# Kernel tuning notes

Hardware: AMD Instinct MI355X
Metric: run time of the kernel (lower is better)

Reference implementation:

```python
import jax, jax.numpy as jnp
import numpy as np

N_NODES = 50000
N_EDGES = 800000
D = 128


def gin_layer(x, edge_index, edge_attr, ee1, ee2, W1, b1, W2, b2):
    # PyG default flow source_to_target: x_j = x[edge_index[0]], aggregate at edge_index[1]
    src, dst = edge_index[0], edge_index[1]
    edge_emb = ee1[edge_attr[:, 0]] + ee2[edge_attr[:, 1]]           # [E, D]
    msg = x[src] + edge_emb                                          # [E, D]
    aggr = jax.ops.segment_sum(msg, dst, num_segments=x.shape[0])    # [N, D]
    h = jax.nn.relu(aggr @ W1 + b1)                                  # [N, 2D]
    return h @ W2 + b2                                               # [N, out]


def setup_inputs() -> dict:
    key = jax.random.key(0)
    ks = jax.random.split(key, 16)
    s = 1.0 / np.sqrt(D)
    inp = {
        "x": jax.random.normal(ks[0], (N_NODES, D), jnp.float32),
        "edge_index": jax.random.randint(ks[1], (2, N_EDGES), 0, N_NODES, dtype=jnp.int32),
        "edge_attr": jax.random.randint(ks[2], (N_EDGES, 2), 0, 3, dtype=jnp.int32),
        "ee1_0": jax.random.normal(ks[3], (6, D), jnp.float32) * s,
        "ee2_0": jax.random.normal(ks[4], (3, D), jnp.float32) * s,
        "W1_0": jax.random.normal(ks[5], (D, 2 * D), jnp.float32) * s,
        "b1_0": jnp.zeros((2 * D,), jnp.float32),
        "W2_0": jax.random.normal(ks[6], (2 * D, D), jnp.float32) * s,
        "b2_0": jnp.zeros((D,), jnp.float32),
        "ee1_1": jax.random.normal(ks[7], (6, D), jnp.float32) * s,
        "ee2_1": jax.random.normal(ks[8], (3, D), jnp.float32) * s,
        "W1_1": jax.random.normal(ks[9], (D, 2 * D), jnp.float32) * s,
        "b1_1": jnp.zeros((2 * D,), jnp.float32),
        "W2_1": jax.random.normal(ks[10], (2 * D, D), jnp.float32) * s,
        "b2_1": jnp.zeros((D,), jnp.float32),
    }
    return inp


def reference(x, edge_index, edge_attr, ee1_0, ee2_0, W1_0, b1_0, W2_0, b2_0,
              ee1_1, ee2_1, W1_1, b1_1, W2_1, b2_1):
    h = gin_layer(x, edge_index, edge_attr, ee1_0, ee2_0, W1_0, b1_0, W2_0, b2_0)
    h = jax.nn.relu(h)  # activation between GNN layers
    out = gin_layer(h, edge_index, edge_attr, ee1_1, ee2_1, W1_1, b1_1, W2_1, b2_1)
    return out  # jk='last'
```

## Files before the change

### kernel.cpp

```cpp
#include <hip/hip_runtime.h>

typedef __attribute__((ext_vector_type(8))) short s16x8;
typedef __attribute__((ext_vector_type(4))) float f32x4;
typedef unsigned short u16;
typedef unsigned char u8;
typedef unsigned long long u64;

#define D_FEAT 128
#define TILE1 4096

__device__ __forceinline__ u16 f2bf(float f) {
    unsigned u = __builtin_bit_cast(unsigned, f);
    u = u + 0x7fffu + ((u >> 16) & 1u);
    return (u16)(u >> 16);
}

__global__ __launch_bounds__(256) void prep_kernel(
        const float4* __restrict__ X4, u16* __restrict__ xb, int n4, int nbA,
        const int* __restrict__ dst, int* __restrict__ ghist, int E, int nb1, int bins,
        const float* __restrict__ ee1_0, const float* __restrict__ ee2_0,
        const float* __restrict__ ee1_1, const float* __restrict__ ee2_1,
        float* __restrict__ emb,
        const float* __restrict__ W1_0, const float* __restrict__ W2_0,
        const float* __restrict__ W1_1, const float* __restrict__ W2_1,
        u16* __restrict__ wout) {
    __shared__ int h[256];
    const int t = threadIdx.x;
    int b = blockIdx.x;

    if (b < nbA) {
        for (int i = b * 256 + t; i < n4; i += nbA * 256) {
            float4 v = X4[i];
            uint2 p;
            p.x = (unsigned)f2bf(v.x) | ((unsigned)f2bf(v.y) << 16);
            p.y = (unsigned)f2bf(v.z) | ((unsigned)f2bf(v.w) << 16);
            *(uint2*)(xb + (size_t)i * 4) = p;
        }
        return;
    }
    b -= nbA;
    if (b < nb1) {
        h[t] = 0;
        __syncthreads();
        const int base = b * TILE1;
        #pragma unroll
        for (int j = 0; j < TILE1 / 256; ++j) {
            int e = base + j * 256 + t;
            if (e < E) atomicAdd(&h[dst[e] >> 8], 1);
        }
        __syncthreads();
        if (t < bins) ghist[t * nb1 + b] = h[t];
        return;
    }
    b -= nb1;
    if (b < 18) {
        int gi = b * 256 + t;
        int layer = gi / 2304;
        int rem = gi - layer * 2304;
        int code = rem >> 7;
        int d = rem & 127;
        int a0 = code / 3, a1 = code - a0 * 3;
        const float* e1 = layer ? ee1_1 : ee1_0;
        const float* e2 = layer ? ee2_1 : ee2_0;
        emb[layer * 2304 + code * 128 + d] = e1[a0 * 128 + d] + e2[a1 * 128 + d];
        return;
    }
    b -= 18;
    {
        int mat = b >> 7;
        const float* s = (mat == 0) ? W1_0 : (mat == 1) ? W2_0 : (mat == 2) ? W1_1 : W2_1;
        u16* d = wout + mat * 32768;
        int o = (b & 127) * 256 + t;
        int n, k;
        if (mat & 1) {
            const int tt = o >> 12, kb = (o >> 9) & 7, lane = (o >> 3) & 63, j = o & 7;
            n = tt * 16 + (lane & 15);
            k = kb * 32 + (lane >> 4) * 8 + j;
            d[o] = f2bf(s[k * 128 + n]);
        } else {
            const int tt = o >> 11, kb = (o >> 9) & 3, lane = (o >> 3) & 63, j = o & 7;
            n = tt * 16 + (lane & 15);
            k = kb * 32 + (lane >> 4) * 8 + j;
            d[o] = f2bf(s[k * 256 + n]);
        }
    }
}

__global__ __launch_bounds__(256) void scan1a_kernel(int* __restrict__ ghist,
                                                     int* __restrict__ btot, int nb1) {
    __shared__ int wt[4];
    const int t = threadIdx.x, lane = t & 63, wid = t >> 6;
    const int bin = blockIdx.x;
    const int v = (t < nb1) ? ghist[bin * nb1 + t] : 0;
    int s = v;
    #pragma unroll
    for (int off = 1; off < 64; off <<= 1) {
        int u = __shfl_up(s, off, 64);
        if (lane >= off) s += u;
    }
    if (lane == 63) wt[wid] = s;
    __syncthreads();
    int add = 0;
    #pragma unroll
    for (int w = 0; w < 4; ++w) add += (w < wid) ? wt[w] : 0;
    s += add;
    if (t < nb1) ghist[bin * nb1 + t] = s - v;
    if (t == 255) btot[bin] = s;
}

__global__ __launch_bounds__(256) void scatter1_kernel(const int* __restrict__ src,
                                                       const int* __restrict__ dst,
                                                       const int* __restrict__ eattr,
                                                       const int* __restrict__ ghist,
                                                       const int* __restrict__ btot,
                                                       u64* __restrict__ buf1,
                                                       int E, int nb1, int bins) {
    __shared__ int lofs[256];
    __shared__ int wt[4];
    const int t = threadIdx.x, lane = t & 63, wid = t >> 6;
    const int v = (t < bins) ? btot[t] : 0;
    int s = v;
    #pragma unroll
    for (int off = 1; off < 64; off <<= 1) {
        int u = __shfl_up(s, off, 64);
        if (lane >= off) s += u;
    }
    if (lane == 63) wt[wid] = s;
    __syncthreads();
    int add = 0;
    #pragma unroll
    for (int w = 0; w < 4; ++w) add += (w < wid) ? wt[w] : 0;
    s += add;
    if (t < bins) lofs[t] = (s - v) + ghist[t * nb1 + blockIdx.x];
    __syncthreads();

    const int base = blockIdx.x * TILE1;
    #pragma unroll
    for (int j = 0; j < TILE1 / 256; ++j) {
        int e = base + j * 256 + t;
        if (e < E) {
            int d = dst[e];
            int2 at = ((const int2*)eattr)[e];
            unsigned pay = (unsigned)src[e] | ((unsigned)(at.x * 3 + at.y) << 16);
            int pos = atomicAdd(&lofs[d >> 8], 1);
            buf1[pos] = ((u64)(unsigned)d << 32) | pay;
        }
    }
}

__global__ __launch_bounds__(1024) void bucket2_kernel(const u64* __restrict__ buf1,
                                                       const int* __restrict__ btot,
                                                       int* __restrict__ row_start,
                                                       unsigned* __restrict__ edges,
                                                       unsigned* __restrict__ countsw,
                                                       int N, int bins) {
    __shared__ int cnt[256];
    __shared__ int cur[256];
    __shared__ int wts[4];
    __shared__ unsigned ccnt[256 * 18];
    __shared__ int sb[2];
    const int t = threadIdx.x, lane = t & 63, wid = t >> 6;
    const int bin = blockIdx.x;

    int v0 = 0, s0 = 0;
    if (t < 256) {
        v0 = (t < bins) ? btot[t] : 0;
        s0 = v0;
        #pragma unroll
        for (int off = 1; off < 64; off <<= 1) {
            int u = __shfl_up(s0, off, 64);
            if (lane >= off) s0 += u;
        }
        if (lane == 63) wts[wid] = s0;
        cnt[t] = 0;
    }
    for (int i = t; i < 256 * 18; i += 1024) ccnt[i] = 0;
    __syncthreads();
    if (t < 256) {
        int add = 0;
        #pragma unroll
        for (int w = 0; w < 4; ++w) add += (w < wid) ? wts[w] : 0;
        s0 += add;
        if (t == bin) { sb[0] = s0 - v0; sb[1] = s0; }
    }
    __syncthreads();
    const int lo = sb[0], hi = sb[1];

    for (int i = lo + t; i < hi; i += 1024)
        atomicAdd(&cnt[(int)(buf1[i] >> 32) & 255], 1);
    __syncthreads();

    int v1 = 0, s1 = 0;
    if (t < 256) {
        v1 = cnt[t];
        s1 = v1;
        #pragma unroll
        for (int off = 1; off < 64; off <<= 1) {
            int u = __shfl_up(s1, off, 64);
            if (lane >= off) s1 += u;
        }
        if (lane == 63) wts[wid] = s1;
    }
    __syncthreads();
    if (t < 256) {
        int add = 0;
        #pragma unroll
        for (int w = 0; w < 4; ++w) add += (w < wid) ? wts[w] : 0;
        s1 += add;
        const int g = bin * 256 + t;
        if (g < N) row_start[g + 1] = lo + s1;
        cur[t] = s1 - v1;
        if (bin == 0 && t == 0) row_start[0] = 0;
    }
    __syncthreads();

    for (int i = lo + t; i < hi; i += 1024) {
        u64 rec = buf1[i];
        const int local = (int)(rec >> 32) & 255;
        int loc = atomicAdd(&cur[local], 1);
        edges[lo + loc] = (unsigned)rec;
        atomicAdd(&ccnt[local * 18 + ((unsigned)rec >> 16)], 1);
    }
    __syncthreads();

    if (t < 256) {
        const int g = bin * 256 + t;
        if (g < N) {
            unsigned w[5] = {0, 0, 0, 0, 0};
            #pragma unroll
            for (int c = 0; c < 18; ++c)
                w[c >> 2] |= ccnt[t * 18 + c] << (8 * (c & 3));
            #pragma unroll
            for (int k = 0; k < 5; ++k)
                countsw[(size_t)g * 5 + k] = w[k];
        }
    }
}

__global__ __launch_bounds__(256) void aggregate_kernel(const u16* __restrict__ X,
                                                        const int* __restrict__ row_start,
                                                        const unsigned* __restrict__ edges,
                                                        const float* __restrict__ emb,
                                                        const unsigned* __restrict__ countsw,
                                                        u16* __restrict__ A, int N) {
    __shared__ float semb[18 * 128];
    for (int i = threadIdx.x; i < 18 * 128; i += 256) semb[i] = emb[i];
    __syncthreads();
    const int lane = threadIdx.x & 63;
    const int wstart = blockIdx.x * 4 + (threadIdx.x >> 6);
    const int wstride = gridDim.x * 4;
    const float2* sem2 = (const float2*)semb;

    for (int node = wstart; node < N; node += wstride) {
        unsigned cw[5];
        #pragma unroll
        for (int k = 0; k < 5; ++k) cw[k] = countsw[(size_t)node * 5 + k];

        int s = __builtin_amdgcn_readfirstlane(row_start[node]);
        const int e = __builtin_amdgcn_readfirstlane(row_start[node + 1]);
        float a0 = 0.f, a1 = 0.f;

        while (s < e) {
            const int take = (e - s < 64) ? (e - s) : 64;
            unsigned pl = edges[s + (lane < take ? lane : 0)];
            #pragma unroll
            for (int c = 0; c < 4; ++c) {
                const int cb = c * 16;
                if (cb < take) {
                    unsigned ps[16];
                    unsigned xv[16];
                    #pragma unroll
                    for (int j = 0; j < 16; ++j)
                        ps[j] = __builtin_amdgcn_readlane(pl, cb + j);
                    #pragma unroll
                    for (int j = 0; j < 16; ++j)
                        xv[j] = *(const unsigned*)(X + (ps[j] & 0xFFFFu) * D_FEAT + lane * 2);
                    #pragma unroll
                    for (int j = 0; j < 16; ++j) {
                        const float m = (cb + j < take) ? 1.f : 0.f;
                        a0 += m * __builtin_bit_cast(float, xv[j] << 16);
                        a1 += m * __builtin_bit_cast(float, xv[j] & 0xFFFF0000u);
                    }
                }
            }
            s += take;
        }

        #pragma unroll
        for (int w = 0; w < 5; ++w) {
            #pragma unroll
            for (int b = 0; b < 4; ++b) {
                const int code = w * 4 + b;
                if (code < 18) {
                    const float cf = (float)((cw[w] >> (8 * b)) & 255u);
                    float2 ev = sem2[code * 64 + lane];
                    a0 += cf * ev.x;
                    a1 += cf * ev.y;
                }
            }
        }

        unsigned outp = (unsigned)f2bf(a0) | ((unsigned)f2bf(a1) << 16);
        *(unsigned*)(A + (size_t)node * D_FEAT + lane * 2) = outp;
    }
}

template <bool RELU2, bool OUTF32>
__global__ __launch_bounds__(256, 2) void mlp_kernel(const u16* __restrict__ A,
                                                     const u16* __restrict__ F1,
                                                     const float* __restrict__ bias1,
                                                     const u16* __restrict__ F2,
                                                     const float* __restrict__ bias2,
                                                     void* __restrict__ C, int M) {
    __shared__ __align__(16) u16 hh[64 * 256];
    const int tid = threadIdx.x;
    const int w = tid >> 6;
    const int lane = tid & 63;
    const int m16 = lane & 15;
    const int quad = lane >> 4;
    const int row0 = blockIdx.x * 64;

    s16x8 af[4][4];
    #pragma unroll
    for (int rf = 0; rf < 4; ++rf) {
        const int arow = row0 + rf * 16 + m16;
        const bool ok = arow < M;
        #pragma unroll
        for (int kb = 0; kb < 4; ++kb)
            af[rf][kb] = ok ? *(const s16x8*)(A + (size_t)arow * 128 + kb * 32 + quad * 8)
                            : s16x8{};
    }

    s16x8 b1f[4][4];
    #pragma unroll
    for (int ct = 0; ct < 4; ++ct)
        #pragma unroll
        for (int kb = 0; kb < 4; ++kb)
            b1f[ct][kb] = *(const s16x8*)(F1 + (size_t)(((w * 4 + ct) * 4 + kb) * 64 + lane) * 8);

    float b1v[4];
    #pragma unroll
    for (int ct = 0; ct < 4; ++ct) b1v[ct] = bias1[(w * 4 + ct) * 16 + m16];

    f32x4 acc[4][4];
    #pragma unroll
    for (int rf = 0; rf < 4; ++rf)
        #pragma unroll
        for (int ct = 0; ct < 4; ++ct) acc[rf][ct] = f32x4{0, 0, 0, 0};
    #pragma unroll
    for (int kb = 0; kb < 4; ++kb)
        #pragma unroll
        for (int rf = 0; rf < 4; ++rf)
            #pragma unroll
            for (int ct = 0; ct < 4; ++ct)
                acc[rf][ct] = __builtin_amdgcn_mfma_f32_16x16x32_bf16(af[rf][kb], b1f[ct][kb],
                                                                     acc[rf][ct], 0, 0, 0);

    #pragma unroll
    for (int rf = 0; rf < 4; ++rf) {
        #pragma unroll
        for (int ct = 0; ct < 4; ++ct) {
            const int col = (w * 4 + ct) * 16 + m16;
            #pragma unroll
            for (int r = 0; r < 4; ++r) {
                const int lr = quad * 4 + r;
                float v = acc[rf][ct][r] + b1v[ct];
                v = v > 0.f ? v : 0.f;
                hh[((rf * 16 + lr) * 256 + col) ^ ((lr & 7) << 3)] = f2bf(v);
            }
        }
    }

    s16x8 b2f[2][8];
    #pragma unroll
    for (int ct2 = 0; ct2 < 2; ++ct2)
        #pragma unroll
        for (int kb = 0; kb < 8; ++kb)
            b2f[ct2][kb] = *(const s16x8*)(F2 + (size_t)(((w * 2 + ct2) * 8 + kb) * 64 + lane) * 8);
    float b2v[2];
    #pragma unroll
    for (int ct2 = 0; ct2 < 2; ++ct2) b2v[ct2] = bias2[(w * 2 + ct2) * 16 + m16];

    __syncthreads();

    f32x4 acc2[4][2];
    #pragma unroll
    for (int rf = 0; rf < 4; ++rf)
        #pragma unroll
        for (int ct2 = 0; ct2 < 2; ++ct2) acc2[rf][ct2] = f32x4{0, 0, 0, 0};
    #pragma unroll
    for (int kb = 0; kb < 8; ++kb) {
        s16x8 haf[4];
        #pragma unroll
        for (int rf = 0; rf < 4; ++rf)
            haf[rf] = *(const s16x8*)(hh + (((rf * 16 + m16) * 256 + kb * 32 + quad * 8)
                                            ^ ((m16 & 7) << 3)));
        #pragma unroll
        for (int rf = 0; rf < 4; ++rf)
            #pragma unroll
            for (int ct2 = 0; ct2 < 2; ++ct2)
                acc2[rf][ct2] = __builtin_amdgcn_mfma_f32_16x16x32_bf16(haf[rf], b2f[ct2][kb],
                                                                       acc2[rf][ct2], 0, 0, 0);
    }

    #pragma unroll
    for (int rf = 0; rf < 4; ++rf) {
        #pragma unroll
        for (int ct2 = 0; ct2 < 2; ++ct2) {
            const int col = (w * 2 + ct2) * 16 + m16;
            #pragma unroll
            for (int r = 0; r < 4; ++r) {
                const int row = row0 + rf * 16 + quad * 4 + r;
                if (row < M) {
                    float v = acc2[rf][ct2][r] + b2v[ct2];
                    if (RELU2) v = v > 0.f ? v : 0.f;
                    if (OUTF32) ((float*)C)[(size_t)row * 128 + col] = v;
                    else        ((u16*)C)[(size_t)row * 128 + col] = f2bf(v);
                }
            }
        }
    }
}

extern "C" void kernel_launch(void* const* d_in, const int* in_sizes, int n_in,
                              void* d_out, int out_size, void* d_ws, size_t ws_size,
                              hipStream_t stream) {
    const int N = in_sizes[0] / D_FEAT;
    const int E = in_sizes[1] / 2;

    const float* x    = (const float*)d_in[0];
    const int* eidx   = (const int*)d_in[1];
    const int* eattr  = (const int*)d_in[2];
    const float* ee1_0 = (const float*)d_in[3];
    const float* ee2_0 = (const float*)d_in[4];
    const float* W1_0  = (const float*)d_in[5];
    const float* b1_0  = (const float*)d_in[6];
    const float* W2_0  = (const float*)d_in[7];
    const float* b2_0  = (const float*)d_in[8];
    const float* ee1_1 = (const float*)d_in[9];
    const float* ee2_1 = (const float*)d_in[10];
    const float* W1_1  = (const float*)d_in[11];
    const float* b1_1  = (const float*)d_in[12];
    const float* W2_1  = (const float*)d_in[13];
    const float* b2_1  = (const float*)d_in[14];

    const int nb1  = (E + TILE1 - 1) / TILE1;
    const int bins = (N + 255) / 256;

    char* ws = (char*)d_ws;
    size_t off = 0;
    auto alloc = [&](size_t bytes) { size_t o = off; off = (off + bytes + 255) & ~(size_t)255; return o; };
    size_t o_rowstart = alloc((size_t)(N + 4) * 4);
    size_t o_edges    = alloc((size_t)E * 4);
    size_t o_ghist    = alloc((size_t)bins * nb1 * 4);
    size_t o_btot     = alloc((size_t)bins * 4);
    size_t o_counts   = alloc((size_t)N * 20);
    size_t o_emb      = alloc(2 * 18 * 128 * 4);
    size_t o_wt       = alloc(4 * 32768 * 2);
    size_t o_aa       = alloc((size_t)N * D_FEAT * 2);

    int*      row_start = (int*)(ws + o_rowstart);
    unsigned* edges     = (unsigned*)(ws + o_edges);
    int*      ghist     = (int*)(ws + o_ghist);
    int*      btot      = (int*)(ws + o_btot);
    unsigned* countsw   = (unsigned*)(ws + o_counts);
    float*    emb       = (float*)(ws + o_emb);
    u16*      F1_0      = (u16*)(ws + o_wt);
    u16*      F2_0      = F1_0 + 32768;
    u16*      F1_1      = F2_0 + 32768;
    u16*      F2_1      = F1_1 + 32768;
    u16*      AA        = (u16*)(ws + o_aa);
    u64*      buf1      = (u64*)(ws + o_aa);

    u16* X2 = (u16*)d_out;
    u16* xb = (u16*)d_out + (size_t)N * D_FEAT;

    const int nt = (N + 63) / 64;
    const int n4 = N * D_FEAT / 4;
    const int nbA = 1024;
    const int aggB = 2048;

    prep_kernel<<<nbA + nb1 + 18 + 512, 256, 0, stream>>>(
        (const float4*)x, xb, n4, nbA,
        eidx + E, ghist, E, nb1, bins,
        ee1_0, ee2_0, ee1_1, ee2_1, emb,
        W1_0, W2_0, W1_1, W2_1, F1_0);

    scan1a_kernel<<<bins, 256, 0, stream>>>(ghist, btot, nb1);
    scatter1_kernel<<<nb1, 256, 0, stream>>>(eidx, eidx + E, eattr, ghist, btot, buf1, E, nb1, bins);
    bucket2_kernel<<<bins, 1024, 0, stream>>>(buf1, btot, row_start, edges, countsw, N, bins);

    aggregate_kernel<<<aggB, 256, 0, stream>>>(xb, row_start, edges, emb, countsw, AA, N);
    mlp_kernel<true, false><<<nt, 256, 0, stream>>>(AA, F1_0, b1_0, F2_0, b2_0, X2, N);

    aggregate_kernel<<<aggB, 256, 0, stream>>>(X2, row_start, edges, emb + 18 * 128, countsw, AA, N);
    mlp_kernel<false, true><<<nt, 256, 0, stream>>>(AA, F1_1, b1_1, F2_1, b2_1, d_out, N);
}
```

Measured before the change: 256.9 us.

## Fuse neighbor aggregation into the MLP kernel via shared-memory tile

Merges the aggregate and MLP kernels so each 64-node block gathers and sums neighbor features into an LDS tile, then runs both MFMA GEMMs directly from it. This removes the round-trip of the aggregated bf16 matrix through global memory and two kernel launches per layer. The layer-1 output now lives in workspace instead of the output buffer. In exchange, the gather loses the grid-stride load balancing and is tied to the MLP block's occupancy (launch bounds 2 blocks per CU, with extra LDS for the tile), so latency hiding for the irregular gathers may drop.

```diff
diff --git a/kernel.cpp b/kernel.cpp
--- a/kernel.cpp
+++ b/kernel.cpp
@@ -237,81 +237,18 @@
     }
 }
 
-__global__ __launch_bounds__(256) void aggregate_kernel(const u16* __restrict__ X,
-                                                        const int* __restrict__ row_start,
-                                                        const unsigned* __restrict__ edges,
-                                                        const float* __restrict__ emb,
-                                                        const unsigned* __restrict__ countsw,
-                                                        u16* __restrict__ A, int N) {
+template <bool RELU2, bool OUTF32>
+__global__ __launch_bounds__(256, 2) void fused_kernel(
+        const u16* __restrict__ X,
+        const int* __restrict__ row_start,
+        const unsigned* __restrict__ edges,
+        const float* __restrict__ emb,
+        const unsigned* __restrict__ countsw,
+        const u16* __restrict__ F1, const float* __restrict__ bias1,
+        const u16* __restrict__ F2, const float* __restrict__ bias2,
+        void* __restrict__ C, int N) {
     __shared__ float semb[18 * 128];
-    for (int i = threadIdx.x; i < 18 * 128; i += 256) semb[i] = emb[i];
-    __syncthreads();
-    const int lane = threadIdx.x & 63;
-    const int wstart = blockIdx.x * 4 + (threadIdx.x >> 6);
-    const int wstride = gridDim.x * 4;
-    const float2* sem2 = (const float2*)semb;
-
-    for (int node = wstart; node < N; node += wstride) {
-        unsigned cw[5];
-        #pragma unroll
-        for (int k = 0; k < 5; ++k) cw[k] = countsw[(size_t)node * 5 + k];
-
-        int s = __builtin_amdgcn_readfirstlane(row_start[node]);
-        const int e = __builtin_amdgcn_readfirstlane(row_start[node + 1]);
-        float a0 = 0.f, a1 = 0.f;
-
-        while (s < e) {
-            const int take = (e - s < 64) ? (e - s) : 64;
-            unsigned pl = edges[s + (lane < take ? lane : 0)];
-            #pragma unroll
-            for (int c = 0; c < 4; ++c) {
-                const int cb = c * 16;
-                if (cb < take) {
-                    unsigned ps[16];
-                    unsigned xv[16];
-                    #pragma unroll
-                    for (int j = 0; j < 16; ++j)
-                        ps[j] = __builtin_amdgcn_readlane(pl, cb + j);
-                    #pragma unroll
-                    for (int j = 0; j < 16; ++j)
-                        xv[j] = *(const unsigned*)(X + (ps[j] & 0xFFFFu) * D_FEAT + lane * 2);
-                    #pragma unroll
-                    for (int j = 0; j < 16; ++j) {
-                        const float m = (cb + j < take) ? 1.f : 0.f;
-                        a0 += m * __builtin_bit_cast(float, xv[j] << 16);
-                        a1 += m * __builtin_bit_cast(float, xv[j] & 0xFFFF0000u);
-                    }
-                }
-            }
-            s += take;
-        }
-
-        #pragma unroll
-        for (int w = 0; w < 5; ++w) {
-            #pragma unroll
-            for (int b = 0; b < 4; ++b) {
-                const int code = w * 4 + b;
-                if (code < 18) {
-                    const float cf = (float)((cw[w] >> (8 * b)) & 255u);
-                    float2 ev = sem2[code * 64 + lane];
-                    a0 += cf * ev.x;
-                    a1 += cf * ev.y;
-                }
-            }
-        }
-
-        unsigned outp = (unsigned)f2bf(a0) | ((unsigned)f2bf(a1) << 16);
-        *(unsigned*)(A + (size_t)node * D_FEAT + lane * 2) = outp;
-    }
-}
-
-template <bool RELU2, bool OUTF32>
-__global__ __launch_bounds__(256, 2) void mlp_kernel(const u16* __restrict__ A,
-                                                     const u16* __restrict__ F1,
-                                                     const float* __restrict__ bias1,
-                                                     const u16* __restrict__ F2,
-                                                     const float* __restrict__ bias2,
-                                                     void* __restrict__ C, int M) {
+    __shared__ __align__(16) u16 at[64 * 128];
     __shared__ __align__(16) u16 hh[64 * 256];
     const int tid = threadIdx.x;
     const int w = tid >> 6;
@@ -320,15 +257,65 @@
     const int quad = lane >> 4;
     const int row0 = blockIdx.x * 64;
 
-    s16x8 af[4][4];
-    #pragma unroll
-    for (int rf = 0; rf < 4; ++rf) {
-        const int arow = row0 + rf * 16 + m16;
-        const bool ok = arow < M;
-        #pragma unroll
-        for (int kb = 0; kb < 4; ++kb)
-            af[rf][kb] = ok ? *(const s16x8*)(A + (size_t)arow * 128 + kb * 32 + quad * 8)
-                            : s16x8{};
+    for (int i = tid; i < 18 * 128; i += 256) semb[i] = emb[i];
+    __syncthreads();
+    const float2* sem2 = (const float2*)semb;
+
+    for (int i = 0; i < 16; ++i) {
+        const int row = w * 16 + i;
+        const int node = row0 + row;
+        unsigned outp = 0u;
+        if (node < N) {
+            unsigned cw[5];
+            #pragma unroll
+            for (int k = 0; k < 5; ++k) cw[k] = countsw[(size_t)node * 5 + k];
+
+            int s = __builtin_amdgcn_readfirstlane(row_start[node]);
+            const int e = __builtin_amdgcn_readfirstlane(row_start[node + 1]);
+            float a0 = 0.f, a1 = 0.f;
+
+            while (s < e) {
+                const int take = (e - s < 64) ? (e - s) : 64;
+                unsigned pl = edges[s + (lane < take ? lane : 0)];
+                #pragma unroll
+                for (int c = 0; c < 4; ++c) {
+                    const int cb = c * 16;
+                    if (cb < take) {
+                        unsigned ps[16];
+                        unsigned xv[16];
+                        #pragma unroll
+                        for (int j = 0; j < 16; ++j)
+                            ps[j] = __builtin_amdgcn_readlane(pl, cb + j);
+                        #pragma unroll
+                        for (int j = 0; j < 16; ++j)
+                            xv[j] = *(const unsigned*)(X + (ps[j] & 0xFFFFu) * D_FEAT + lane * 2);
+                        #pragma unroll
+                        for (int j = 0; j < 16; ++j) {
+                            const float m = (cb + j < take) ? 1.f : 0.f;
+                            a0 += m * __builtin_bit_cast(float, xv[j] << 16);
+                            a1 += m * __builtin_bit_cast(float, xv[j] & 0xFFFF0000u);
+                        }
+                    }
+                }
+                s += take;
+            }
+
+            #pragma unroll
+            for (int ww = 0; ww < 5; ++ww) {
+                #pragma unroll
+                for (int b = 0; b < 4; ++b) {
+                    const int code = ww * 4 + b;
+                    if (code < 18) {
+                        const float cf = (float)((cw[ww] >> (8 * b)) & 255u);
+                        float2 ev = sem2[code * 64 + lane];
+                        a0 += cf * ev.x;
+                        a1 += cf * ev.y;
+                    }
+                }
+            }
+            outp = (unsigned)f2bf(a0) | ((unsigned)f2bf(a1) << 16);
+        }
+        *(unsigned*)(at + (((row * 128 + lane * 2) ^ ((row & 7) << 3)))) = outp;
     }
 
     s16x8 b1f[4][4];
@@ -337,24 +324,41 @@
         #pragma unroll
         for (int kb = 0; kb < 4; ++kb)
             b1f[ct][kb] = *(const s16x8*)(F1 + (size_t)(((w * 4 + ct) * 4 + kb) * 64 + lane) * 8);
-
     float b1v[4];
     #pragma unroll
     for (int ct = 0; ct < 4; ++ct) b1v[ct] = bias1[(w * 4 + ct) * 16 + m16];
 
+    __syncthreads();
+
     f32x4 acc[4][4];
     #pragma unroll
     for (int rf = 0; rf < 4; ++rf)
         #pragma unroll
         for (int ct = 0; ct < 4; ++ct) acc[rf][ct] = f32x4{0, 0, 0, 0};
     #pragma unroll
-    for (int kb = 0; kb < 4; ++kb)
-        #pragma unroll
-        for (int rf = 0; rf < 4; ++rf)
+    for (int rf = 0; rf < 4; ++rf) {
+        s16x8 af[4];
+        #pragma unroll
+        for (int kb = 0; kb < 4; ++kb)
+            af[kb] = *(const s16x8*)(at + ((((rf * 16 + m16) * 128) + kb * 32 + quad * 8)
+                                           ^ ((m16 & 7) << 3)));
+        #pragma unroll
+        for (int kb = 0; kb < 4; ++kb)
             #pragma unroll
             for (int ct = 0; ct < 4; ++ct)
-                acc[rf][ct] = __builtin_amdgcn_mfma_f32_16x16x32_bf16(af[rf][kb], b1f[ct][kb],
+                acc[rf][ct] = __builtin_amdgcn_mfma_f32_16x16x32_bf16(af[kb], b1f[ct][kb],
                                                                      acc[rf][ct], 0, 0, 0);
+    }
+
+    s16x8 b2f[2][8];
+    #pragma unroll
+    for (int ct2 = 0; ct2 < 2; ++ct2)
+        #pragma unroll
+        for (int kb = 0; kb < 8; ++kb)
+            b2f[ct2][kb] = *(const s16x8*)(F2 + (size_t)(((w * 2 + ct2) * 8 + kb) * 64 + lane) * 8);
+    float b2v[2];
+    #pragma unroll
+    for (int ct2 = 0; ct2 < 2; ++ct2) b2v[ct2] = bias2[(w * 2 + ct2) * 16 + m16];
 
     #pragma unroll
     for (int rf = 0; rf < 4; ++rf) {
@@ -370,17 +374,6 @@
             }
         }
     }
-
-    s16x8 b2f[2][8];
-    #pragma unroll
-    for (int ct2 = 0; ct2 < 2; ++ct2)
-        #pragma unroll
-        for (int kb = 0; kb < 8; ++kb)
-            b2f[ct2][kb] = *(const s16x8*)(F2 + (size_t)(((w * 2 + ct2) * 8 + kb) * 64 + lane) * 8);
-    float b2v[2];
-    #pragma unroll
-    for (int ct2 = 0; ct2 < 2; ++ct2) b2v[ct2] = bias2[(w * 2 + ct2) * 16 + m16];
-
     __syncthreads();
 
     f32x4 acc2[4][2];
@@ -411,7 +404,7 @@
             #pragma unroll
             for (int r = 0; r < 4; ++r) {
                 const int row = row0 + rf * 16 + quad * 4 + r;
-                if (row < M) {
+                if (row < N) {
                     float v = acc2[rf][ct2][r] + b2v[ct2];
                     if (RELU2) v = v > 0.f ? v : 0.f;
                     if (OUTF32) ((float*)C)[(size_t)row * 128 + col] = v;
@@ -457,7 +450,9 @@
     size_t o_counts   = alloc((size_t)N * 20);
     size_t o_emb      = alloc(2 * 18 * 128 * 4);
     size_t o_wt       = alloc(4 * 32768 * 2);
-    size_t o_aa       = alloc((size_t)N * D_FEAT * 2);
+    size_t big = (size_t)E * 8;
+    size_t x2b = (size_t)N * D_FEAT * 2;
+    size_t o_big      = alloc(big > x2b ? big : x2b);
 
     int*      row_start = (int*)(ws + o_rowstart);
     unsigned* edges     = (unsigned*)(ws + o_edges);
@@ -469,16 +464,14 @@
     u16*      F2_0      = F1_0 + 32768;
     u16*      F1_1      = F2_0 + 32768;
     u16*      F2_1      = F1_1 + 32768;
-    u16*      AA        = (u16*)(ws + o_aa);
-    u64*      buf1      = (u64*)(ws + o_aa);
-
-    u16* X2 = (u16*)d_out;
+    u64*      buf1      = (u64*)(ws + o_big);
+    u16*      X2        = (u16*)(ws + o_big);
+
     u16* xb = (u16*)d_out + (size_t)N * D_FEAT;
 
     const int nt = (N + 63) / 64;
     const int n4 = N * D_FEAT / 4;
     const int nbA = 1024;
-    const int aggB = 2048;
 
     prep_kernel<<<nbA + nb1 + 18 + 512, 256, 0, stream>>>(
         (const float4*)x, xb, n4, nbA,
@@ -490,9 +483,9 @@
     scatter1_kernel<<<nb1, 256, 0, stream>>>(eidx, eidx + E, eattr, ghist, btot, buf1, E, nb1, bins);
     bucket2_kernel<<<bins, 1024, 0, stream>>>(buf1, btot, row_start, edges, countsw, N, bins);
 
-    aggregate_kernel<<<aggB, 256, 0, stream>>>(xb, row_start, edges, emb, countsw, AA, N);
-    mlp_kernel<true, false><<<nt, 256, 0, stream>>>(AA, F1_0, b1_0, F2_0, b2_0, X2, N);
-
-    aggregate_kernel<<<aggB, 256, 0, stream>>>(X2, row_start, edges, emb + 18 * 128, countsw, AA, N);
-    mlp_kernel<false, true><<<nt, 256, 0, stream>>>(AA, F1_1, b1_1, F2_1, b2_1, d_out, N);
-}
+    fused_kernel<true, false><<<nt, 256, 0, stream>>>(
+        xb, row_start, edges, emb, countsw, F1_0, b1_0, F2_0, b2_0, X2, N);
+
+    fused_kernel<false, true><<<nt, 256, 0, stream>>>(
+        X2, row_start, edges, emb + 18 * 128, countsw, F1_1, b1_1, F2_1, b2_1, d_out, N);
+}
```

New measurement: 287.5 us. +11.9%, slower.
